# Performance work log

Measured on AMD Instinct MI355X. Metric: run time of the kernel, lower is better.

## Reference

```python
import jax, jax.numpy as jnp
import numpy as np

N, E, G, DIM, XF, EF = 50000, 800000, 512, 64, 28, 3

def setup_inputs():
    key = jax.random.key(0)
    ks = iter(jax.random.split(key, 64))
    def nrm(shape, scale=0.1):
        return jax.random.normal(next(ks), shape, dtype=jnp.float32) * scale
    inp = {}
    inp["x"] = jax.random.normal(next(ks), (N, XF), dtype=jnp.float32)
    inp["edge_attr"] = jax.random.normal(next(ks), (E, EF), dtype=jnp.float32)
    # conv1: bond_encoder 3->28->28, mlp 28->28->DIM
    inp["c1_be1"] = nrm((EF, XF)); inp["c1_be2"] = nrm((XF, XF))
    inp["c1_m1"] = nrm((XF, XF)); inp["c1_m2"] = nrm((XF, DIM))
    inp["c1_eps"] = jnp.zeros((1,), jnp.float32)
    # conv2: bond_encoder 3->DIM->DIM, mlp DIM->DIM->DIM
    inp["c2_be1"] = nrm((EF, DIM)); inp["c2_be2"] = nrm((DIM, DIM))
    inp["c2_m1"] = nrm((DIM, DIM)); inp["c2_m2"] = nrm((DIM, DIM))
    inp["c2_eps"] = jnp.zeros((1,), jnp.float32)
    # conv3 (reused for layer 4, as in the source)
    inp["c3_be1"] = nrm((EF, DIM)); inp["c3_be2"] = nrm((DIM, DIM))
    inp["c3_m1"] = nrm((DIM, DIM)); inp["c3_m2"] = nrm((DIM, DIM))
    inp["c3_eps"] = jnp.zeros((1,), jnp.float32)
    for i in (1, 2, 3, 4):
        inp["bn%d_g" % i] = jnp.ones((DIM,), jnp.float32) + nrm((DIM,), 0.01)
        inp["bn%d_b" % i] = nrm((DIM,), 0.01)
        inp["bn%d_m" % i] = nrm((DIM,), 0.1)
        inp["bn%d_v" % i] = jnp.ones((DIM,), jnp.float32) + jax.random.uniform(next(ks), (DIM,), dtype=jnp.float32)
    inp["fc1_w"] = nrm((4 * DIM, DIM)); inp["fc1_b"] = jnp.zeros((DIM,), jnp.float32)
    inp["fc2_w"] = nrm((DIM, DIM)); inp["fc2_b"] = jnp.zeros((DIM,), jnp.float32)
    inp["fc3_w"] = nrm((DIM, DIM)); inp["fc3_b"] = jnp.zeros((DIM,), jnp.float32)
    inp["fc4_w"] = nrm((DIM, 1)); inp["fc4_b"] = jnp.zeros((1,), jnp.float32)
    inp["edge_index"] = jax.random.randint(next(ks), (2, E), 0, N, dtype=jnp.int32)
    inp["batch"] = jnp.sort(jax.random.randint(next(ks), (N,), 0, G, dtype=jnp.int32))
    return inp

def reference(x, edge_attr, c1_be1, c1_be2, c1_m1, c1_m2, c1_eps, c2_be1, c2_be2, c2_m1, c2_m2, c2_eps, c3_be1, c3_be2, c3_m1, c3_m2, c3_eps, bn1_g, bn1_b, bn1_m, bn1_v, bn2_g, bn2_b, bn2_m, bn2_v, bn3_g, bn3_b, bn3_m, bn3_v, bn4_g, bn4_b, bn4_m, bn4_v, fc1_w, fc1_b, fc2_w, fc2_b, fc3_w, fc3_b, fc4_w, fc4_b, edge_index, batch):
    n = x.shape[0]
    src, dst = edge_index[0], edge_index[1]
    def gin(h, be1, be2, m1, m2, eps):
        e = jnp.maximum(edge_attr @ be1, 0.0) @ be2            # bond encoder [E, d]
        msg = jnp.maximum(h[src] + e, 0.0)                     # edge gather + relu
        agg = jax.ops.segment_sum(msg, dst, num_segments=n)    # scatter-add aggregate
        z = (1.0 + eps) * h + agg
        return jnp.maximum(z @ m1, 0.0) @ m2                   # node MLP
    def bn(h, g, b, m, v):                                     # BatchNorm1d (eval)
        return (h - m) * (g * jax.lax.rsqrt(v + 1e-5)) + b
    x1 = bn(jnp.maximum(gin(x,  c1_be1, c1_be2, c1_m1, c1_m2, c1_eps), 0.0), bn1_g, bn1_b, bn1_m, bn1_v)
    x2 = bn(jnp.maximum(gin(x1, c2_be1, c2_be2, c2_m1, c2_m2, c2_eps), 0.0), bn2_g, bn2_b, bn2_m, bn2_v)
    x3 = bn(jnp.maximum(gin(x2, c3_be1, c3_be2, c3_m1, c3_m2, c3_eps), 0.0), bn3_g, bn3_b, bn3_m, bn3_v)
    x4 = bn(jnp.maximum(gin(x3, c3_be1, c3_be2, c3_m1, c3_m2, c3_eps), 0.0), bn4_g, bn4_b, bn4_m, bn4_v)  # conv3 reused, faithful to source
    cat = jnp.concatenate([x1, x2, x3, x4], axis=-1)           # [N, 4*DIM]
    cnt = jax.ops.segment_sum(jnp.ones((n,), cat.dtype), batch, num_segments=G)
    pooled = jax.ops.segment_sum(cat, batch, num_segments=G) / jnp.maximum(cnt, 1.0)[:, None]
    h = jnp.maximum(pooled @ fc1_w + fc1_b, 0.0)
    h = jnp.maximum(h @ fc2_w + fc2_b, 0.0)
    h = jnp.maximum(h @ fc3_w + fc3_b, 0.0)
    return (h @ fc4_w + fc4_b).reshape(-1)
```

## Files before the change

### kernel.cpp

```cpp
#include <hip/hip_runtime.h>


typedef __attribute__((ext_vector_type(8))) short short8v;
typedef __attribute__((ext_vector_type(4))) float float4v;

__device__ __forceinline__ unsigned short f2bf(float f) {
  unsigned u = __float_as_uint(f);
  u += 0x7fff + ((u >> 16) & 1);
  return (unsigned short)(u >> 16);
}
__device__ __forceinline__ float bf2f(unsigned short s) {
  return __uint_as_float(((unsigned)s) << 16);
}
__device__ __forceinline__ float4v mfma16(short8v a, short8v b, float4v c) {
  return __builtin_amdgcn_mfma_f32_16x16x32_bf16(a, b, c, 0, 0, 0);
}

__global__ __launch_bounds__(256) void prep_kernel(
    const float* c1be2, const float* c2be2, const float* c3be2,
    const float* c1m1, const float* c2m1, const float* c3m1,
    const float* c1m2, const float* c2m2, const float* c3m2,
    const float* c1be1, const float* c2be1, const float* c3be1,
    unsigned short* FB, float* B1P) {
  int job = blockIdx.x;
  if (job < 9) {
    const float* W = nullptr; int ldw = 0, kmax = 0, nmax = 0, NT = 0, KT = 0;
    switch (job) {
      case 0: W = c1be2; ldw = 28; kmax = 28; nmax = 28; NT = 2; KT = 1; break;
      case 1: W = c2be2; ldw = 64; kmax = 64; nmax = 64; NT = 4; KT = 2; break;
      case 2: W = c3be2; ldw = 64; kmax = 64; nmax = 64; NT = 4; KT = 2; break;
      case 3: W = c1m1;  ldw = 28; kmax = 28; nmax = 28; NT = 2; KT = 1; break;
      case 4: W = c2m1;  ldw = 64; kmax = 64; nmax = 64; NT = 4; KT = 2; break;
      case 5: W = c3m1;  ldw = 64; kmax = 64; nmax = 64; NT = 4; KT = 2; break;
      case 6: W = c1m2;  ldw = 64; kmax = 28; nmax = 64; NT = 4; KT = 1; break;
      case 7: W = c2m2;  ldw = 64; kmax = 64; nmax = 64; NT = 4; KT = 2; break;
      case 8: W = c3m2;  ldw = 64; kmax = 64; nmax = 64; NT = 4; KT = 2; break;
    }
    unsigned short* out = FB + (size_t)job * 4096;
    int total = NT * KT * 512;
    for (int i = threadIdx.x; i < total; i += 256) {
      int fi = i >> 9, l = (i >> 3) & 63, j = i & 7;
      int kt = fi % KT, nt = fi / KT;
      int k = kt * 32 + (l >> 4) * 8 + j;
      int n = nt * 16 + (l & 15);
      float w = (k < kmax && n < nmax) ? W[k * ldw + n] : 0.f;
      out[i] = f2bf(w);
    }
  } else {
    int b = job - 9;
    const float* be1 = (b == 0) ? c1be1 : (b == 1) ? c2be1 : c3be1;
    int DE = (b == 0) ? 28 : 64;
    float* out = B1P + (size_t)b * (64 * 48);
    for (int i = threadIdx.x; i < 64 * 48; i += 256) {
      int l = i / 48, r = i % 48;
      int c = r / 16, kk = r % 16;
      int kt = kk >> 3, j = kk & 7;
      int k = kt * 32 + ((l >> 4) & 3) * 8 + j;
      out[i] = (k < DE) ? be1[c * DE + k] : 0.f;
    }
  }
}


__global__ void hist_kernel(const int* __restrict__ idx, int* __restrict__ cnt, int n) {
  int i = blockIdx.x * blockDim.x + threadIdx.x;
  int stride = gridDim.x * blockDim.x;
  for (; i < n; i += stride) atomicAdd(&cnt[idx[i]], 1);
}

__global__ void fill_perm_kernel(const int* __restrict__ srcs, const int* __restrict__ dsts,
                                 const float* __restrict__ eattr, int* __restrict__ cursor,
                                 int* __restrict__ src_s, float4* __restrict__ attr_s,
                                 int n) {
  int i = blockIdx.x * blockDim.x + threadIdx.x;
  int stride = gridDim.x * blockDim.x;
  for (; i < n; i += stride) {
    int d = dsts[i];
    int p = atomicAdd(&cursor[d], 1);
    src_s[p] = srcs[i];
    attr_s[p] = make_float4(eattr[i * 3 + 0], eattr[i * 3 + 1], eattr[i * 3 + 2], 0.f);
  }
}

__global__ __launch_bounds__(256) void block_reduce_kernel(
    const int* __restrict__ cnt, int* __restrict__ bsum, int n) {
  __shared__ int s[256];
  int i = blockIdx.x * 256 + threadIdx.x;
  s[threadIdx.x] = (i < n) ? cnt[i] : 0;
  __syncthreads();
  for (int d = 128; d > 0; d >>= 1) {
    if (threadIdx.x < d) s[threadIdx.x] += s[threadIdx.x + d];
    __syncthreads();
  }
  if (threadIdx.x == 0) bsum[blockIdx.x] = s[0];
}

__global__ __launch_bounds__(256) void bsum_scan_kernel(int* __restrict__ bsum, int nb) {
  __shared__ int s[1024];
  for (int i = threadIdx.x; i < 1024; i += 256) s[i] = (i < nb) ? bsum[i] : 0;
  __syncthreads();
  if (threadIdx.x == 0) {
    int acc = 0;
    for (int i = 0; i < nb; i++) { int t = s[i]; s[i] = acc; acc += t; }
  }
  __syncthreads();
  for (int i = threadIdx.x; i < nb; i += 256) bsum[i] = s[i];
}

__global__ __launch_bounds__(256) void scan_apply_kernel(
    const int* __restrict__ cnt, const int* __restrict__ bsum,
    int* __restrict__ offs, int* __restrict__ cursor, int n) {
  __shared__ int s[256];
  int b = blockIdx.x;
  int i = b * 256 + threadIdx.x;
  int v = (i < n) ? cnt[i] : 0;
  s[threadIdx.x] = v;
  __syncthreads();
  for (int d = 1; d < 256; d <<= 1) {
    int t = (threadIdx.x >= d) ? s[threadIdx.x - d] : 0;
    __syncthreads();
    s[threadIdx.x] += t;
    __syncthreads();
  }
  int excl = s[threadIdx.x] - v + bsum[b];
  if (i < n) { offs[i] = excl; cursor[i] = excl; }
  if (i == n - 1) offs[n] = excl + v;
}

__global__ void boundary_kernel(const int* __restrict__ batch, int* __restrict__ goff,
                                int n, int G) {
  int g = blockIdx.x * blockDim.x + threadIdx.x;
  if (g > G) return;
  int lo = 0, hi = n;
  while (lo < hi) {
    int mid = (lo + hi) >> 1;
    if (batch[mid] < g) lo = mid + 1; else hi = mid;
  }
  goff[g] = lo;
}

template <int DE>
__global__ __launch_bounds__(256) void bond_kernel(
    const float4* __restrict__ attr_s, const float* __restrict__ b1p,
    const unsigned short* __restrict__ be2f, unsigned short* __restrict__ ebond, int E) {
  constexpr int KT = (DE + 31) / 32;
  constexpr int NT = (DE + 15) / 16;
  constexpr int RB = KT * 32;
  int lane = threadIdx.x & 63;
  int nc = lane & 15, rr = (lane >> 4) * 4;
  int gw = (blockIdx.x * blockDim.x + threadIdx.x) >> 6;
  int nw = (gridDim.x * blockDim.x) >> 6;

  float b1v[3][KT * 8];
#pragma unroll
  for (int c = 0; c < 3; c++)
#pragma unroll
    for (int kk = 0; kk < KT * 8; kk++)
      b1v[c][kk] = b1p[lane * 48 + c * 16 + (kk >> 3) * 8 + (kk & 7)];

  short8v bfrag[NT][KT];
#pragma unroll
  for (int nt = 0; nt < NT; nt++)
#pragma unroll
    for (int kt = 0; kt < KT; kt++)
      bfrag[nt][kt] = *(const short8v*)(be2f + ((nt * KT + kt) * 64 + lane) * 8);

  int ntiles = (E + 15) >> 4;
  for (int tile = gw; tile < ntiles; tile += nw) {
    int j0 = tile << 4;
    int je = j0 + nc;
    float4 a = attr_s[min(je, E - 1)];
    short8v af[KT];
#pragma unroll
    for (int kt = 0; kt < KT; kt++)
#pragma unroll
      for (int j = 0; j < 8; j++) {
        int kk = kt * 8 + j;
        float t = fmaxf(fmaf(a.x, b1v[0][kk], fmaf(a.y, b1v[1][kk], a.z * b1v[2][kk])), 0.f);
        af[kt][j] = (short)f2bf(t);
      }
    float4v acc[NT];
#pragma unroll
    for (int nt = 0; nt < NT; nt++) {
      acc[nt] = (float4v){0.f, 0.f, 0.f, 0.f};
#pragma unroll
      for (int kt = 0; kt < KT; kt++) acc[nt] = mfma16(af[kt], bfrag[nt][kt], acc[nt]);
    }
#pragma unroll
    for (int nt = 0; nt < NT; nt++)
#pragma unroll
      for (int r = 0; r < 4; r++) {
        int row = j0 + rr + r;
        if (row < E) ebond[(size_t)row * RB + nt * 16 + nc] = f2bf(acc[nt][r]);
      }
  }
}

template <int DH, int RB>
__global__ __launch_bounds__(256) void agg_kernel(
    const float* __restrict__ h, const unsigned short* __restrict__ eb,
    const float* __restrict__ epsp, const int* __restrict__ src_sorted,
    const int* __restrict__ offs, float* __restrict__ zout, int n_nodes) {
  int wid = (blockIdx.x * blockDim.x + threadIdx.x) >> 6;
  int nw = (gridDim.x * blockDim.x) >> 6;
  int lane = threadIdx.x & 63;
  float eps1 = 1.f + epsp[0];
  const bool hl = (DH == 64) || (lane < DH);
  const bool el = (RB == 64) || (lane < RB);
  for (int v = wid; v < n_nodes; v += nw) {
    float acc = hl ? eps1 * h[(size_t)v * DH + lane] : 0.f;
    int j = offs[v], e1 = offs[v + 1];
    for (; j + 8 <= e1; j += 8) {
      int ss[8];
      float eb8[8], hh[8];
#pragma unroll
      for (int q = 0; q < 8; q++) ss[q] = src_sorted[j + q];
#pragma unroll
      for (int q = 0; q < 8; q++)
        eb8[q] = el ? bf2f(eb[(size_t)(j + q) * RB + lane]) : 0.f;
#pragma unroll
      for (int q = 0; q < 8; q++) hh[q] = hl ? h[(size_t)ss[q] * DH + lane] : 0.f;
#pragma unroll
      for (int q = 0; q < 8; q++) acc += fmaxf(hh[q] + eb8[q], 0.f);
    }
    for (; j + 4 <= e1; j += 4) {
      int ss[4];
      float eb4[4], hh[4];
#pragma unroll
      for (int q = 0; q < 4; q++) ss[q] = src_sorted[j + q];
#pragma unroll
      for (int q = 0; q < 4; q++)
        eb4[q] = el ? bf2f(eb[(size_t)(j + q) * RB + lane]) : 0.f;
#pragma unroll
      for (int q = 0; q < 4; q++) hh[q] = hl ? h[(size_t)ss[q] * DH + lane] : 0.f;
#pragma unroll
      for (int q = 0; q < 4; q++) acc += fmaxf(hh[q] + eb4[q], 0.f);
    }
    for (; j < e1; j++) {
      int s = src_sorted[j];
      float b = el ? bf2f(eb[(size_t)j * RB + lane]) : 0.f;
      float hs = hl ? h[(size_t)s * DH + lane] : 0.f;
      acc += fmaxf(hs + b, 0.f);
    }
    if (el) zout[(size_t)v * RB + lane] = acc;
  }
}

template <int DIN>
__global__ __launch_bounds__(256) void node_mfma_kernel(
    const float* __restrict__ z, const unsigned short* __restrict__ m1f_g,
    const unsigned short* __restrict__ m2f_g, const float* __restrict__ bng,
    const float* __restrict__ bnb, const float* __restrict__ bnm,
    const float* __restrict__ bnv, float* __restrict__ xout, int n_nodes) {
  constexpr int KT = (DIN + 31) / 32;
  constexpr int NTH = (DIN + 15) / 16;
  constexpr int ZR = KT * 32;
  constexpr int LROW = 64 * 2 + 16;
  __shared__ __attribute__((aligned(16))) char lds_all[4 * 16 * LROW];
  char* yl = lds_all + (threadIdx.x >> 6) * (16 * LROW);
  int lane = threadIdx.x & 63;
  int nc = lane & 15, kg = lane >> 4, rr = kg * 4;
  int gw = (blockIdx.x * blockDim.x + threadIdx.x) >> 6;
  int nw = (gridDim.x * blockDim.x) >> 6;

  short8v m1f[NTH][KT], m2f[4][KT];
#pragma unroll
  for (int nt = 0; nt < NTH; nt++)
#pragma unroll
    for (int kt = 0; kt < KT; kt++)
      m1f[nt][kt] = *(const short8v*)(m1f_g + ((nt * KT + kt) * 64 + lane) * 8);
#pragma unroll
  for (int nt = 0; nt < 4; nt++)
#pragma unroll
    for (int kt = 0; kt < KT; kt++)
      m2f[nt][kt] = *(const short8v*)(m2f_g + ((nt * KT + kt) * 64 + lane) * 8);

  float scv[4], shv[4];
#pragma unroll
  for (int nt = 0; nt < 4; nt++) {
    int f = nt * 16 + nc;
    float sc = bng[f] * rsqrtf(bnv[f] + 1e-5f);
    scv[nt] = sc;
    shv[nt] = bnb[f] - bnm[f] * sc;
  }

  int ntiles = (n_nodes + 15) >> 4;
  for (int tile = gw; tile < ntiles; tile += nw) {
    int v0 = tile << 4;
    int vr = min(v0 + nc, n_nodes - 1);
    short8v af[KT];
#pragma unroll
    for (int kt = 0; kt < KT; kt++) {
      const float* zp = z + (size_t)vr * ZR + kt * 32 + kg * 8;
      float4 z0 = *(const float4*)(zp);
      float4 z1 = *(const float4*)(zp + 4);
      af[kt][0] = (short)f2bf(z0.x); af[kt][1] = (short)f2bf(z0.y);
      af[kt][2] = (short)f2bf(z0.z); af[kt][3] = (short)f2bf(z0.w);
      af[kt][4] = (short)f2bf(z1.x); af[kt][5] = (short)f2bf(z1.y);
      af[kt][6] = (short)f2bf(z1.z); af[kt][7] = (short)f2bf(z1.w);
    }
    float4v acch[NTH];
#pragma unroll
    for (int nt = 0; nt < NTH; nt++) {
      acch[nt] = (float4v){0.f, 0.f, 0.f, 0.f};
#pragma unroll
      for (int kt = 0; kt < KT; kt++) acch[nt] = mfma16(af[kt], m1f[nt][kt], acch[nt]);
    }
#pragma unroll
    for (int nt = 0; nt < NTH; nt++)
#pragma unroll
      for (int r = 0; r < 4; r++)
        *(unsigned short*)(yl + (rr + r) * LROW + (nt * 16 + nc) * 2) =
            f2bf(fmaxf(acch[nt][r], 0.f));
    asm volatile("" ::: "memory");
    short8v af2[KT];
#pragma unroll
    for (int kt = 0; kt < KT; kt++)
      af2[kt] = *(const short8v*)(yl + nc * LROW + kg * 16 + kt * 64);
    float4v acco[4];
#pragma unroll
    for (int nt = 0; nt < 4; nt++) {
      acco[nt] = (float4v){0.f, 0.f, 0.f, 0.f};
#pragma unroll
      for (int kt = 0; kt < KT; kt++) acco[nt] = mfma16(af2[kt], m2f[nt][kt], acco[nt]);
    }
#pragma unroll
    for (int nt = 0; nt < 4; nt++)
#pragma unroll
      for (int r = 0; r < 4; r++) {
        int v = v0 + rr + r;
        if (v < n_nodes)
          xout[(size_t)v * 64 + nt * 16 + nc] =
              fmaf(fmaxf(acco[nt][r], 0.f), scv[nt], shv[nt]);
      }
    asm volatile("" ::: "memory");
  }
}

__global__ __launch_bounds__(256) void pool_kernel(
    const float* __restrict__ x1, const float* __restrict__ x2,
    const float* __restrict__ x3, const float* __restrict__ x4,
    const int* __restrict__ goff, float* __restrict__ pooled, int G) {
  int g = blockIdx.x;
  int c = threadIdx.x;
  int sel = c >> 6, f = c & 63;
  const float* x = (sel == 0) ? x1 : (sel == 1) ? x2 : (sel == 2) ? x3 : x4;
  int s = goff[g], e = goff[g + 1];
  float acc = 0.f;
  for (int v = s; v < e; v++) acc += x[(size_t)v * 64 + f];
  float cnt = (float)(e - s);
  pooled[g * 256 + c] = acc / fmaxf(cnt, 1.0f);
}

__global__ __launch_bounds__(64) void head_kernel(
    const float* __restrict__ pooled,
    const float* __restrict__ w1, const float* __restrict__ b1,
    const float* __restrict__ w2, const float* __restrict__ b2,
    const float* __restrict__ w3, const float* __restrict__ b3,
    const float* __restrict__ w4, const float* __restrict__ b4,
    float* __restrict__ out, int G) {
  int g = blockIdx.x;
  int lane = threadIdx.x;
  __shared__ float sh[256];
  for (int i = lane; i < 256; i += 64) sh[i] = pooled[g * 256 + i];
  __syncthreads();
  float h1 = b1[lane];
#pragma unroll 8
  for (int i = 0; i < 256; i++) h1 = fmaf(sh[i], w1[i * 64 + lane], h1);
  h1 = fmaxf(h1, 0.f);
  __syncthreads();
  sh[lane] = h1;
  __syncthreads();
  float h2 = b2[lane];
#pragma unroll
  for (int i = 0; i < 64; i++) h2 = fmaf(sh[i], w2[i * 64 + lane], h2);
  h2 = fmaxf(h2, 0.f);
  __syncthreads();
  sh[lane] = h2;
  __syncthreads();
  float h3 = b3[lane];
#pragma unroll
  for (int i = 0; i < 64; i++) h3 = fmaf(sh[i], w3[i * 64 + lane], h3);
  h3 = fmaxf(h3, 0.f);
  float p = h3 * w4[lane];
  for (int d = 32; d > 0; d >>= 1) p += __shfl_down(p, d);
  if (lane == 0) out[g] = p + b4[0];
}


extern "C" void kernel_launch(void* const* d_in, const int* in_sizes, int n_in,
                              void* d_out, int out_size, void* d_ws, size_t ws_size,
                              hipStream_t stream) {
  const float* x      = (const float*)d_in[0];
  const float* eattr  = (const float*)d_in[1];
  const float* c1_be1 = (const float*)d_in[2];
  const float* c1_be2 = (const float*)d_in[3];
  const float* c1_m1  = (const float*)d_in[4];
  const float* c1_m2  = (const float*)d_in[5];
  const float* c1_eps = (const float*)d_in[6];
  const float* c2_be1 = (const float*)d_in[7];
  const float* c2_be2 = (const float*)d_in[8];
  const float* c2_m1  = (const float*)d_in[9];
  const float* c2_m2  = (const float*)d_in[10];
  const float* c2_eps = (const float*)d_in[11];
  const float* c3_be1 = (const float*)d_in[12];
  const float* c3_be2 = (const float*)d_in[13];
  const float* c3_m1  = (const float*)d_in[14];
  const float* c3_m2  = (const float*)d_in[15];
  const float* c3_eps = (const float*)d_in[16];
  const float* bn_g[4] = {(const float*)d_in[17], (const float*)d_in[21],
                          (const float*)d_in[25], (const float*)d_in[29]};
  const float* bn_b[4] = {(const float*)d_in[18], (const float*)d_in[22],
                          (const float*)d_in[26], (const float*)d_in[30]};
  const float* bn_m[4] = {(const float*)d_in[19], (const float*)d_in[23],
                          (const float*)d_in[27], (const float*)d_in[31]};
  const float* bn_v[4] = {(const float*)d_in[20], (const float*)d_in[24],
                          (const float*)d_in[28], (const float*)d_in[32]};
  const float* fc1_w = (const float*)d_in[33];
  const float* fc1_b = (const float*)d_in[34];
  const float* fc2_w = (const float*)d_in[35];
  const float* fc2_b = (const float*)d_in[36];
  const float* fc3_w = (const float*)d_in[37];
  const float* fc3_b = (const float*)d_in[38];
  const float* fc4_w = (const float*)d_in[39];
  const float* fc4_b = (const float*)d_in[40];
  const int* eidx  = (const int*)d_in[41];
  const int* batch = (const int*)d_in[42];

  const int N = in_sizes[0] / 28;
  const int E = in_sizes[1] / 3;
  const int G = out_size;
  const int* src = eidx;
  const int* dst = eidx + E;
  float* outf = (float*)d_out;

  char* p = (char*)d_ws;
  auto alloc = [&](size_t bytes) {
    char* r = p;
    p += (bytes + 255) & ~(size_t)255;
    return r;
  };
  const int NBLK = (N + 255) / 256;
  int* counts   = (int*)alloc((size_t)N * 4);
  int* offs     = (int*)alloc((size_t)(N + 1) * 4);
  int* cursor   = (int*)alloc((size_t)N * 4);
  int* bsum     = (int*)alloc((size_t)NBLK * 4);
  int* goff     = (int*)alloc((size_t)(G + 1) * 4);
  int* src_s    = (int*)alloc((size_t)E * 4);
  float4* attr_s = (float4*)alloc((size_t)E * 16);
  unsigned short* FB = (unsigned short*)alloc(9 * 4096 * 2);
  float* B1P    = (float*)alloc(3 * 64 * 48 * 4);
  unsigned short* ebond = (unsigned short*)alloc((size_t)E * 64 * 2);
  float* zbuf   = (float*)alloc((size_t)N * 64 * 4);
  float* x1     = (float*)alloc((size_t)N * 64 * 4);
  float* x2     = (float*)alloc((size_t)N * 64 * 4);
  float* x3     = (float*)alloc((size_t)N * 64 * 4);
  float* x4     = (float*)alloc((size_t)N * 64 * 4);
  float* pooled = (float*)alloc((size_t)G * 256 * 4);
  (void)ws_size; (void)n_in;

  prep_kernel<<<12, 256, 0, stream>>>(c1_be2, c2_be2, c3_be2, c1_m1, c2_m1, c3_m1,
                                      c1_m2, c2_m2, c3_m2, c1_be1, c2_be1, c3_be1,
                                      FB, B1P);
  hipMemsetAsync(counts, 0, (size_t)N * 4, stream);
  hist_kernel<<<1024, 256, 0, stream>>>(dst, counts, E);
  boundary_kernel<<<(G + 128) / 128, 128, 0, stream>>>(batch, goff, N, G);
  block_reduce_kernel<<<NBLK, 256, 0, stream>>>(counts, bsum, N);
  bsum_scan_kernel<<<1, 256, 0, stream>>>(bsum, NBLK);
  scan_apply_kernel<<<NBLK, 256, 0, stream>>>(counts, bsum, offs, cursor, N);
  fill_perm_kernel<<<1024, 256, 0, stream>>>(src, dst, eattr, cursor, src_s, attr_s, E);

  unsigned short* FB_be2[3] = {FB + 0 * 4096, FB + 1 * 4096, FB + 2 * 4096};
  unsigned short* FB_m1[3]  = {FB + 3 * 4096, FB + 4 * 4096, FB + 5 * 4096};
  unsigned short* FB_m2[3]  = {FB + 6 * 4096, FB + 7 * 4096, FB + 8 * 4096};
  float* B1[3] = {B1P, B1P + 64 * 48, B1P + 2 * 64 * 48};

  dim3 blk(256);
  bond_kernel<28><<<1024, blk, 0, stream>>>(attr_s, B1[0], FB_be2[0], ebond, E);
  agg_kernel<28, 32><<<2048, blk, 0, stream>>>(x, ebond, c1_eps, src_s, offs, zbuf, N);
  node_mfma_kernel<28><<<512, blk, 0, stream>>>(zbuf, FB_m1[0], FB_m2[0], bn_g[0],
                                                bn_b[0], bn_m[0], bn_v[0], x1, N);
  bond_kernel<64><<<1024, blk, 0, stream>>>(attr_s, B1[1], FB_be2[1], ebond, E);
  agg_kernel<64, 64><<<2048, blk, 0, stream>>>(x1, ebond, c2_eps, src_s, offs, zbuf, N);
  node_mfma_kernel<64><<<512, blk, 0, stream>>>(zbuf, FB_m1[1], FB_m2[1], bn_g[1],
                                                bn_b[1], bn_m[1], bn_v[1], x2, N);
  bond_kernel<64><<<1024, blk, 0, stream>>>(attr_s, B1[2], FB_be2[2], ebond, E);
  agg_kernel<64, 64><<<2048, blk, 0, stream>>>(x2, ebond, c3_eps, src_s, offs, zbuf, N);
  node_mfma_kernel<64><<<512, blk, 0, stream>>>(zbuf, FB_m1[2], FB_m2[2], bn_g[2],
                                                bn_b[2], bn_m[2], bn_v[2], x3, N);
  agg_kernel<64, 64><<<2048, blk, 0, stream>>>(x3, ebond, c3_eps, src_s, offs, zbuf, N);
  node_mfma_kernel<64><<<512, blk, 0, stream>>>(zbuf, FB_m1[2], FB_m2[2], bn_g[3],
                                                bn_b[3], bn_m[3], bn_v[3], x4, N);

  pool_kernel<<<G, blk, 0, stream>>>(x1, x2, x3, x4, goff, pooled, G);
  head_kernel<<<G, 64, 0, stream>>>(pooled, fc1_w, fc1_b, fc2_w, fc2_b, fc3_w,
                                    fc3_b, fc4_w, fc4_b, outf, G);
}
```

Before: 619.5 us.

## Fuse bond MLP with edge message aggregation using atomic scatter into z

Removes the materialized bf16 edge-bond buffer and the separate CSR gather aggregation. Each edge tile now computes bond features with MFMA, adds the gathered source node features, applies ReLU, does a small segmented reduction over rows that share a destination, and atomically adds the result into z. A separate init kernel seeds z with (1+eps)*h. This also recomputes the bond features for layer 4 instead of reusing them. It trades the E×64 write and read for float atomics and a dst_s array, with possible contention and nondeterministic summation order.

```diff
diff --git a/kernel.cpp b/kernel.cpp
--- a/kernel.cpp
+++ b/kernel.cpp
@@ -70,14 +70,15 @@
 
 __global__ void fill_perm_kernel(const int* __restrict__ srcs, const int* __restrict__ dsts,
                                  const float* __restrict__ eattr, int* __restrict__ cursor,
-                                 int* __restrict__ src_s, float4* __restrict__ attr_s,
-                                 int n) {
+                                 int* __restrict__ src_s, int* __restrict__ dst_s,
+                                 float4* __restrict__ attr_s, int n) {
   int i = blockIdx.x * blockDim.x + threadIdx.x;
   int stride = gridDim.x * blockDim.x;
   for (; i < n; i += stride) {
     int d = dsts[i];
     int p = atomicAdd(&cursor[d], 1);
     src_s[p] = srcs[i];
+    dst_s[p] = d;
     attr_s[p] = make_float4(eattr[i * 3 + 0], eattr[i * 3 + 1], eattr[i * 3 + 2], 0.f);
   }
 }
@@ -109,7 +110,7 @@
 
 __global__ __launch_bounds__(256) void scan_apply_kernel(
     const int* __restrict__ cnt, const int* __restrict__ bsum,
-    int* __restrict__ offs, int* __restrict__ cursor, int n) {
+    int* __restrict__ cursor, int n) {
   __shared__ int s[256];
   int b = blockIdx.x;
   int i = b * 256 + threadIdx.x;
@@ -123,8 +124,7 @@
     __syncthreads();
   }
   int excl = s[threadIdx.x] - v + bsum[b];
-  if (i < n) { offs[i] = excl; cursor[i] = excl; }
-  if (i == n - 1) offs[n] = excl + v;
+  if (i < n) cursor[i] = excl;
 }
 
 __global__ void boundary_kernel(const int* __restrict__ batch, int* __restrict__ goff,
@@ -139,15 +139,29 @@
   goff[g] = lo;
 }
 
+template <int DH, int RB>
+__global__ __launch_bounds__(256) void init_z_kernel(const float* __restrict__ h,
+                                                     const float* __restrict__ epsp,
+                                                     float* __restrict__ z, int n_nodes) {
+  int i = blockIdx.x * blockDim.x + threadIdx.x;
+  if (i >= n_nodes * RB) return;
+  int v = i / RB, c = i % RB;
+  float val = 0.f;
+  if (DH == RB || c < DH) val = (1.f + epsp[0]) * h[(size_t)v * DH + c];
+  z[i] = val;
+}
+
 template <int DE>
-__global__ __launch_bounds__(256) void bond_kernel(
+__global__ __launch_bounds__(256) void fused_edge_kernel(
     const float4* __restrict__ attr_s, const float* __restrict__ b1p,
-    const unsigned short* __restrict__ be2f, unsigned short* __restrict__ ebond, int E) {
+    const unsigned short* __restrict__ be2f, const float* __restrict__ h,
+    const int* __restrict__ src_s, const int* __restrict__ dst_s,
+    float* __restrict__ z, int E) {
   constexpr int KT = (DE + 31) / 32;
   constexpr int NT = (DE + 15) / 16;
   constexpr int RB = KT * 32;
   int lane = threadIdx.x & 63;
-  int nc = lane & 15, rr = (lane >> 4) * 4;
+  int nc = lane & 15, kg = lane >> 4, rr = kg * 4;
   int gw = (blockIdx.x * blockDim.x + threadIdx.x) >> 6;
   int nw = (gridDim.x * blockDim.x) >> 6;
 
@@ -164,12 +178,15 @@
 #pragma unroll
     for (int kt = 0; kt < KT; kt++)
       bfrag[nt][kt] = *(const short8v*)(be2f + ((nt * KT + kt) * 64 + lane) * 8);
+
+  bool colv[NT];
+#pragma unroll
+  for (int nt = 0; nt < NT; nt++) colv[nt] = (DE == 64) || (nt * 16 + nc < DE);
 
   int ntiles = (E + 15) >> 4;
   for (int tile = gw; tile < ntiles; tile += nw) {
     int j0 = tile << 4;
-    int je = j0 + nc;
-    float4 a = attr_s[min(je, E - 1)];
+    float4 a = attr_s[min(j0 + nc, E - 1)];
     short8v af[KT];
 #pragma unroll
     for (int kt = 0; kt < KT; kt++)
@@ -186,63 +203,45 @@
 #pragma unroll
       for (int kt = 0; kt < KT; kt++) acc[nt] = mfma16(af[kt], bfrag[nt][kt], acc[nt]);
     }
+    int s_r[4], d_r[4];
+    bool rv[4];
+#pragma unroll
+    for (int r = 0; r < 4; r++) {
+      int jr = j0 + rr + r;
+      rv[r] = jr < E;
+      jr = min(jr, E - 1);
+      s_r[r] = src_s[jr];
+      d_r[r] = dst_s[jr];
+    }
+    float m[4][NT];
+#pragma unroll
+    for (int r = 0; r < 4; r++)
+#pragma unroll
+      for (int nt = 0; nt < NT; nt++) {
+        float hv = (rv[r] && colv[nt]) ? h[(size_t)s_r[r] * DE + nt * 16 + nc] : 0.f;
+        m[r][nt] = (rv[r] && colv[nt]) ? fmaxf(hv + acc[nt][r], 0.f) : 0.f;
+      }
+    float racc[NT];
+#pragma unroll
+    for (int nt = 0; nt < NT; nt++) racc[nt] = m[0][nt];
+    int cd = d_r[0];
+#pragma unroll
+    for (int r = 1; r < 4; r++) {
+      if (d_r[r] != cd) {
+#pragma unroll
+        for (int nt = 0; nt < NT; nt++)
+          if (colv[nt]) unsafeAtomicAdd(&z[(size_t)cd * RB + nt * 16 + nc], racc[nt]);
+#pragma unroll
+        for (int nt = 0; nt < NT; nt++) racc[nt] = m[r][nt];
+        cd = d_r[r];
+      } else {
+#pragma unroll
+        for (int nt = 0; nt < NT; nt++) racc[nt] += m[r][nt];
+      }
+    }
 #pragma unroll
     for (int nt = 0; nt < NT; nt++)
-#pragma unroll
-      for (int r = 0; r < 4; r++) {
-        int row = j0 + rr + r;
-        if (row < E) ebond[(size_t)row * RB + nt * 16 + nc] = f2bf(acc[nt][r]);
-      }
-  }
-}
-
-template <int DH, int RB>
-__global__ __launch_bounds__(256) void agg_kernel(
-    const float* __restrict__ h, const unsigned short* __restrict__ eb,
-    const float* __restrict__ epsp, const int* __restrict__ src_sorted,
-    const int* __restrict__ offs, float* __restrict__ zout, int n_nodes) {
-  int wid = (blockIdx.x * blockDim.x + threadIdx.x) >> 6;
-  int nw = (gridDim.x * blockDim.x) >> 6;
-  int lane = threadIdx.x & 63;
-  float eps1 = 1.f + epsp[0];
-  const bool hl = (DH == 64) || (lane < DH);
-  const bool el = (RB == 64) || (lane < RB);
-  for (int v = wid; v < n_nodes; v += nw) {
-    float acc = hl ? eps1 * h[(size_t)v * DH + lane] : 0.f;
-    int j = offs[v], e1 = offs[v + 1];
-    for (; j + 8 <= e1; j += 8) {
-      int ss[8];
-      float eb8[8], hh[8];
-#pragma unroll
-      for (int q = 0; q < 8; q++) ss[q] = src_sorted[j + q];
-#pragma unroll
-      for (int q = 0; q < 8; q++)
-        eb8[q] = el ? bf2f(eb[(size_t)(j + q) * RB + lane]) : 0.f;
-#pragma unroll
-      for (int q = 0; q < 8; q++) hh[q] = hl ? h[(size_t)ss[q] * DH + lane] : 0.f;
-#pragma unroll
-      for (int q = 0; q < 8; q++) acc += fmaxf(hh[q] + eb8[q], 0.f);
-    }
-    for (; j + 4 <= e1; j += 4) {
-      int ss[4];
-      float eb4[4], hh[4];
-#pragma unroll
-      for (int q = 0; q < 4; q++) ss[q] = src_sorted[j + q];
-#pragma unroll
-      for (int q = 0; q < 4; q++)
-        eb4[q] = el ? bf2f(eb[(size_t)(j + q) * RB + lane]) : 0.f;
-#pragma unroll
-      for (int q = 0; q < 4; q++) hh[q] = hl ? h[(size_t)ss[q] * DH + lane] : 0.f;
-#pragma unroll
-      for (int q = 0; q < 4; q++) acc += fmaxf(hh[q] + eb4[q], 0.f);
-    }
-    for (; j < e1; j++) {
-      int s = src_sorted[j];
-      float b = el ? bf2f(eb[(size_t)j * RB + lane]) : 0.f;
-      float hs = hl ? h[(size_t)s * DH + lane] : 0.f;
-      acc += fmaxf(hs + b, 0.f);
-    }
-    if (el) zout[(size_t)v * RB + lane] = acc;
+      if (colv[nt]) unsafeAtomicAdd(&z[(size_t)cd * RB + nt * 16 + nc], racc[nt]);
   }
 }
 
@@ -442,15 +441,14 @@
   };
   const int NBLK = (N + 255) / 256;
   int* counts   = (int*)alloc((size_t)N * 4);
-  int* offs     = (int*)alloc((size_t)(N + 1) * 4);
   int* cursor   = (int*)alloc((size_t)N * 4);
   int* bsum     = (int*)alloc((size_t)NBLK * 4);
   int* goff     = (int*)alloc((size_t)(G + 1) * 4);
   int* src_s    = (int*)alloc((size_t)E * 4);
+  int* dst_s    = (int*)alloc((size_t)E * 4);
   float4* attr_s = (float4*)alloc((size_t)E * 16);
   unsigned short* FB = (unsigned short*)alloc(9 * 4096 * 2);
   float* B1P    = (float*)alloc(3 * 64 * 48 * 4);
-  unsigned short* ebond = (unsigned short*)alloc((size_t)E * 64 * 2);
   float* zbuf   = (float*)alloc((size_t)N * 64 * 4);
   float* x1     = (float*)alloc((size_t)N * 64 * 4);
   float* x2     = (float*)alloc((size_t)N * 64 * 4);
@@ -467,8 +465,9 @@
   boundary_kernel<<<(G + 128) / 128, 128, 0, stream>>>(batch, goff, N, G);
   block_reduce_kernel<<<NBLK, 256, 0, stream>>>(counts, bsum, N);
   bsum_scan_kernel<<<1, 256, 0, stream>>>(bsum, NBLK);
-  scan_apply_kernel<<<NBLK, 256, 0, stream>>>(counts, bsum, offs, cursor, N);
-  fill_perm_kernel<<<1024, 256, 0, stream>>>(src, dst, eattr, cursor, src_s, attr_s, E);
+  scan_apply_kernel<<<NBLK, 256, 0, stream>>>(counts, bsum, cursor, N);
+  fill_perm_kernel<<<1024, 256, 0, stream>>>(src, dst, eattr, cursor, src_s, dst_s,
+                                             attr_s, E);
 
   unsigned short* FB_be2[3] = {FB + 0 * 4096, FB + 1 * 4096, FB + 2 * 4096};
   unsigned short* FB_m1[3]  = {FB + 3 * 4096, FB + 4 * 4096, FB + 5 * 4096};
@@ -476,19 +475,24 @@
   float* B1[3] = {B1P, B1P + 64 * 48, B1P + 2 * 64 * 48};
 
   dim3 blk(256);
-  bond_kernel<28><<<1024, blk, 0, stream>>>(attr_s, B1[0], FB_be2[0], ebond, E);
-  agg_kernel<28, 32><<<2048, blk, 0, stream>>>(x, ebond, c1_eps, src_s, offs, zbuf, N);
+  init_z_kernel<28, 32><<<(N * 32 + 255) / 256, blk, 0, stream>>>(x, c1_eps, zbuf, N);
+  fused_edge_kernel<28><<<1024, blk, 0, stream>>>(attr_s, B1[0], FB_be2[0], x,
+                                                  src_s, dst_s, zbuf, E);
   node_mfma_kernel<28><<<512, blk, 0, stream>>>(zbuf, FB_m1[0], FB_m2[0], bn_g[0],
                                                 bn_b[0], bn_m[0], bn_v[0], x1, N);
-  bond_kernel<64><<<1024, blk, 0, stream>>>(attr_s, B1[1], FB_be2[1], ebond, E);
-  agg_kernel<64, 64><<<2048, blk, 0, stream>>>(x1, ebond, c2_eps, src_s, offs, zbuf, N);
+  init_z_kernel<64, 64><<<(N * 64 + 255) / 256, blk, 0, stream>>>(x1, c2_eps, zbuf, N);
+  fused_edge_kernel<64><<<1024, blk, 0, stream>>>(attr_s, B1[1], FB_be2[1], x1,
+                                                  src_s, dst_s, zbuf, E);
   node_mfma_kernel<64><<<512, blk, 0, stream>>>(zbuf, FB_m1[1], FB_m2[1], bn_g[1],
                                                 bn_b[1], bn_m[1], bn_v[1], x2, N);
-  bond_kernel<64><<<1024, blk, 0, stream>>>(attr_s, B1[2], FB_be2[2], ebond, E);
-  agg_kernel<64, 64><<<2048, blk, 0, stream>>>(x2, ebond, c3_eps, src_s, offs, zbuf, N);
+  init_z_kernel<64, 64><<<(N * 64 + 255) / 256, blk, 0, stream>>>(x2, c3_eps, zbuf, N);
+  fused_edge_kernel<64><<<1024, blk, 0, stream>>>(attr_s, B1[2], FB_be2[2], x2,
+                                                  src_s, dst_s, zbuf, E);
   node_mfma_kernel<64><<<512, blk, 0, stream>>>(zbuf, FB_m1[2], FB_m2[2], bn_g[2],
                                                 bn_b[2], bn_m[2], bn_v[2], x3, N);
-  agg_kernel<64, 64><<<2048, blk, 0, stream>>>(x3, ebond, c3_eps, src_s, offs, zbuf, N);
+  init_z_kernel<64, 64><<<(N * 64 + 255) / 256, blk, 0, stream>>>(x3, c3_eps, zbuf, N);
+  fused_edge_kernel<64><<<1024, blk, 0, stream>>>(attr_s, B1[2], FB_be2[2], x3,
+                                                  src_s, dst_s, zbuf, E);
   node_mfma_kernel<64><<<512, blk, 0, stream>>>(zbuf, FB_m1[2], FB_m2[2], bn_g[3],
                                                 bn_b[3], bn_m[3], bn_v[3], x4, N);
 
```

Measured after the change: 1.062 ms. 71.4% more time.
